# Optimization experiments

Measured on AMD Instinct MI355X. Metric: run time of the kernel, lower is better.

Reference implementation:

```python
import jax, jax.numpy as jnp
import numpy as np

GRID_LO = 32
GRID_HI = 128
NF = 4          # n_features
K = 9           # num_neighbors
NUM_CLASSES = 36
BS = 128
P_LO = GRID_LO * GRID_LO   # 1024
P_HI = GRID_HI * GRID_HI   # 16384


def _knn_neighbor_indices():
    """Replicates cKDTree(lo_coords).query(hi_coords, k=K)[1]: lo grid has
    spacing ratio=grid_hi//grid_lo, hi grid spacing 1; neighbors sorted by
    distance (stable sort -> ties broken by lower linear index)."""
    ratio = GRID_HI // GRID_LO
    lo = np.stack(np.meshgrid(np.arange(GRID_LO) * ratio,
                              np.arange(GRID_LO) * ratio, indexing='ij'),
                  axis=-1).reshape(-1, 2).astype(np.float64)   # (P_LO, 2)
    hi = np.stack(np.meshgrid(np.arange(GRID_HI),
                              np.arange(GRID_HI), indexing='ij'),
                  axis=-1).reshape(-1, 2).astype(np.float64)   # (P_HI, 2)
    d2 = ((hi[:, None, :] - lo[None, :, :]) ** 2).sum(-1)      # (P_HI, P_LO)
    idx = np.argsort(d2, axis=1, kind='stable')[:, :K]          # (P_HI, K)
    return jnp.asarray(idx, dtype=jnp.int32)


def setup_inputs() -> dict:
    key = jax.random.key(0)
    k1, k2, k3, k4, k5 = jax.random.split(key, 5)
    x = jax.random.normal(k1, (BS, NF * P_LO), dtype=jnp.float32)
    cls_ids = jax.random.randint(k2, (BS,), 0, NUM_CLASSES)
    neighbor_indices = _knn_neighbor_indices()                  # (P_HI, K)
    weight_map = jax.random.normal(k3, (NUM_CLASSES, NF, P_HI, K), dtype=jnp.float32) * 0.05
    bias_low = jax.random.normal(k4, (NUM_CLASSES, NF, P_LO), dtype=jnp.float32) * 0.05
    bias_high = jax.random.normal(k5, (NUM_CLASSES, NF, P_HI), dtype=jnp.float32) * 0.05
    return {"x": x, "cls_ids": cls_ids, "neighbor_indices": neighbor_indices,
            "weight_map": weight_map, "bias_low": bias_low, "bias_high": bias_high}


def reference(x, cls_ids, neighbor_indices, weight_map, bias_low, bias_high):
    # x: (BS, NF*P_LO) -> (BS, NF, P_LO)
    y_low = x.reshape(x.shape[0], NF, P_LO)
    y_low_db = y_low - bias_low[cls_ids]                        # (BS, NF, P_LO)
    # gather k=9 lo-res neighbors for every hi-res pixel (all features at once)
    neigh = y_low_db[:, :, neighbor_indices]                    # (BS, NF, P_HI, K)
    weights = weight_map[cls_ids]                               # (BS, NF, P_HI, K)
    out = jnp.einsum('bfpk,bfpk->bfp', neigh, weights)          # weighted sum over k
    out = out + bias_high[cls_ids]                              # (BS, NF, P_HI)
    return out.reshape(x.shape[0], NF, GRID_HI, GRID_HI)
```

## Files before the change

### kernel.cpp

```cpp
#include <hip/hip_runtime.h>

#define BS      128
#define NF      4
#define P_LO    1024
#define P_HI    16384
#define KNN     9
#define THREADS 256
#define CHUNKS  4
#define CHUNK_P (P_HI / CHUNKS)

__global__ __launch_bounds__(THREADS) void rect_up_kernel(
    const float* __restrict__ x,
    const int*   __restrict__ cls_ids,
    const int*   __restrict__ nbr,
    const float* __restrict__ wmap,
    const float* __restrict__ blo,
    const float* __restrict__ bhi,
    float*       __restrict__ out)
{
    __shared__ float ylds[P_LO];

    const int bf    = blockIdx.x / CHUNKS;
    const int chunk = blockIdx.x % CHUNKS;
    const int b     = bf >> 2;
    const int f     = bf & 3;
    const int cls   = cls_ids[b];
    const int tid   = threadIdx.x;

    const float4* xp4  = (const float4*)(x   + (b   * NF + f) * P_LO);
    const float4* blp4 = (const float4*)(blo + (cls * NF + f) * P_LO);
    {
        float4 xv = xp4[tid];
        float4 bv = blp4[tid];
        float4 r;
        r.x = xv.x - bv.x; r.y = xv.y - bv.y;
        r.z = xv.z - bv.z; r.w = xv.w - bv.w;
        ((float4*)ylds)[tid] = r;
    }
    __syncthreads();

    const float* wbase = wmap + (size_t)(cls * NF + f) * P_HI * KNN;
    const float* bhp   = bhi  + (size_t)(cls * NF + f) * P_HI;
    float*       op    = out  + (size_t)(b   * NF + f) * P_HI;

    const int pp_lo = chunk * (CHUNK_P / 2);
    const int pp_hi = pp_lo + (CHUNK_P / 2);

    #pragma unroll 4
    for (int pp = pp_lo + tid; pp < pp_hi; pp += THREADS) {
        const int p0 = pp * 2;

        const int2* ip = (const int2*)(nbr + (size_t)p0 * KNN);
        int idx[18];
        #pragma unroll
        for (int j = 0; j < 9; ++j) {
            int2 v = ip[j];
            idx[2 * j]     = v.x;
            idx[2 * j + 1] = v.y;
        }

        const float2* wp = (const float2*)(wbase + (size_t)p0 * KNN);
        float w[18];
        #pragma unroll
        for (int j = 0; j < 9; ++j) {
            float2 v = wp[j];
            w[2 * j]     = v.x;
            w[2 * j + 1] = v.y;
        }

        float acc0 = 0.f, acc1 = 0.f;
        #pragma unroll
        for (int k = 0; k < 9; ++k) acc0 = fmaf(w[k],     ylds[idx[k]],     acc0);
        #pragma unroll
        for (int k = 0; k < 9; ++k) acc1 = fmaf(w[9 + k], ylds[idx[9 + k]], acc1);

        float2 bh = *(const float2*)(bhp + p0);
        float2 o;
        o.x = acc0 + bh.x;
        o.y = acc1 + bh.y;
        *(float2*)(op + p0) = o;
    }
}

extern "C" void kernel_launch(void* const* d_in, const int* in_sizes, int n_in,
                              void* d_out, int out_size, void* d_ws, size_t ws_size,
                              hipStream_t stream) {
    const float* x    = (const float*)d_in[0];
    const int*   cls  = (const int*)d_in[1];
    const int*   nbr  = (const int*)d_in[2];
    const float* wmap = (const float*)d_in[3];
    const float* blo  = (const float*)d_in[4];
    const float* bhi  = (const float*)d_in[5];
    float*       out  = (float*)d_out;

    dim3 grid(BS * NF * CHUNKS);
    rect_up_kernel<<<grid, THREADS, 0, stream>>>(x, cls, nbr, wmap, blo, bhi, out);
}
```

Baseline: 191.6 us.

## Coalesce neighbor and weight loads via per-wave LDS product staging

Each wave now processes a tile of 128 hi-res pixels, loading the neighbor indices and weights contiguously across lanes and writing the weighted products into a per-wave LDS buffer. Each lane then reads back its two pixels' nine products and sums them. This replaces per-thread strided 72-byte loads with coalesced wave-wide accesses, targeting global memory efficiency. Chunk count doubles to give more blocks. It adds LDS traffic, possible bank conflicts on the strided readback, and a different summation order.

After: 179.4 us. 6.4% less time.

```diff
diff --git a/kernel.cpp b/kernel.cpp
--- a/kernel.cpp
+++ b/kernel.cpp
@@ -6,8 +6,11 @@
 #define P_HI    16384
 #define KNN     9
 #define THREADS 256
-#define CHUNKS  4
+#define CHUNKS  8
 #define CHUNK_P (P_HI / CHUNKS)
+#define TILE_P  128
+#define TILE_F  (TILE_P * KNN)
+#define WAVES   (THREADS / 64)
 
 __global__ __launch_bounds__(THREADS) void rect_up_kernel(
     const float* __restrict__ x,
@@ -19,6 +22,7 @@
     float*       __restrict__ out)
 {
     __shared__ float ylds[P_LO];
+    __shared__ float prod[WAVES][TILE_F];
 
     const int bf    = blockIdx.x / CHUNKS;
     const int chunk = blockIdx.x % CHUNKS;
@@ -26,10 +30,12 @@
     const int f     = bf & 3;
     const int cls   = cls_ids[b];
     const int tid   = threadIdx.x;
+    const int wave  = tid >> 6;
+    const int lane  = tid & 63;
 
-    const float4* xp4  = (const float4*)(x   + (b   * NF + f) * P_LO);
-    const float4* blp4 = (const float4*)(blo + (cls * NF + f) * P_LO);
     {
+        const float4* xp4  = (const float4*)(x   + (b   * NF + f) * P_LO);
+        const float4* blp4 = (const float4*)(blo + (cls * NF + f) * P_LO);
         float4 xv = xp4[tid];
         float4 bv = blp4[tid];
         float4 r;
@@ -42,43 +48,40 @@
     const float* wbase = wmap + (size_t)(cls * NF + f) * P_HI * KNN;
     const float* bhp   = bhi  + (size_t)(cls * NF + f) * P_HI;
     float*       op    = out  + (size_t)(b   * NF + f) * P_HI;
+    float*       pbuf  = prod[wave];
 
-    const int pp_lo = chunk * (CHUNK_P / 2);
-    const int pp_hi = pp_lo + (CHUNK_P / 2);
+    const int tiles = CHUNK_P / TILE_P;
+    for (int t = wave; t < tiles; t += WAVES) {
+        const int    ptile = chunk * CHUNK_P + t * TILE_P;
+        const size_t fbase = (size_t)ptile * KNN;
 
-    #pragma unroll 4
-    for (int pp = pp_lo + tid; pp < pp_hi; pp += THREADS) {
-        const int p0 = pp * 2;
-
-        const int2* ip = (const int2*)(nbr + (size_t)p0 * KNN);
-        int idx[18];
         #pragma unroll
-        for (int j = 0; j < 9; ++j) {
-            int2 v = ip[j];
-            idx[2 * j]     = v.x;
-            idx[2 * j + 1] = v.y;
+        for (int j = 0; j < KNN; ++j) {
+            const int off = j * 128 + 2 * lane;
+            int2   i2 = *(const int2*)  (nbr   + fbase + off);
+            float2 w2 = *(const float2*)(wbase + fbase + off);
+            float2 pr;
+            pr.x = w2.x * ylds[i2.x];
+            pr.y = w2.y * ylds[i2.y];
+            *(float2*)(pbuf + off) = pr;
         }
 
-        const float2* wp = (const float2*)(wbase + (size_t)p0 * KNN);
-        float w[18];
+        float2 r[9];
         #pragma unroll
-        for (int j = 0; j < 9; ++j) {
-            float2 v = wp[j];
-            w[2 * j]     = v.x;
-            w[2 * j + 1] = v.y;
-        }
+        for (int j = 0; j < 9; ++j)
+            r[j] = *(const float2*)(pbuf + lane * 18 + 2 * j);
 
-        float acc0 = 0.f, acc1 = 0.f;
-        #pragma unroll
-        for (int k = 0; k < 9; ++k) acc0 = fmaf(w[k],     ylds[idx[k]],     acc0);
-        #pragma unroll
-        for (int k = 0; k < 9; ++k) acc1 = fmaf(w[9 + k], ylds[idx[9 + k]], acc1);
+        float a0 = r[0].x + r[0].y + r[1].x + r[1].y + r[2].x + r[2].y
+                 + r[3].x + r[3].y + r[4].x;
+        float a1 = r[4].y + r[5].x + r[5].y + r[6].x + r[6].y
+                 + r[7].x + r[7].y + r[8].x + r[8].y;
 
-        float2 bh = *(const float2*)(bhp + p0);
+        const int pp = ptile + 2 * lane;
+        float2 bh = *(const float2*)(bhp + pp);
         float2 o;
-        o.x = acc0 + bh.x;
-        o.y = acc1 + bh.y;
-        *(float2*)(op + p0) = o;
+        o.x = a0 + bh.x;
+        o.y = a1 + bh.y;
+        *(float2*)(op + pp) = o;
     }
 }
 
```

## Group batch rows by class to reuse weight tiles across samples

Applied to the files above, without the earlier changes.

A small pre-kernel buckets batch indices by class id into workspace lists. The main kernel is then launched per (class, feature, pixel tile): it loads that tile's weights and neighbor indices into registers once and loops over every batch row of the class, double-buffering the de-biased low-res input in shared memory. This cuts repeated weight-map reads from once per sample to once per class. The cost is an extra launch, serialized per-sample iterations with a barrier each, and load imbalance or idle blocks when class counts are uneven.

Result: faster. 167.0 us (-12.8%).

```diff
diff --git a/kernel.cpp b/kernel.cpp
--- a/kernel.cpp
+++ b/kernel.cpp
@@ -2,83 +2,115 @@
 
 #define BS      128
 #define NF      4
+#define NC      36
 #define P_LO    1024
 #define P_HI    16384
 #define KNN     9
 #define THREADS 256
-#define CHUNKS  4
-#define CHUNK_P (P_HI / CHUNKS)
+#define TILE_P  512
+#define TILE_F  (TILE_P * KNN)
+#define NTILES  (P_HI / TILE_P)
+#define LIST_OFF 64
+
+__global__ __launch_bounds__(128) void build_lists_kernel(
+    const int* __restrict__ cls_ids, int* __restrict__ ws)
+{
+    __shared__ int cnt[NC];
+    const int t = threadIdx.x;
+    if (t < NC) cnt[t] = 0;
+    __syncthreads();
+    if (t < BS) {
+        int c = cls_ids[t];
+        int pos = atomicAdd(&cnt[c], 1);
+        ws[LIST_OFF + c * BS + pos] = t;
+    }
+    __syncthreads();
+    if (t < NC) ws[t] = cnt[t];
+}
 
 __global__ __launch_bounds__(THREADS) void rect_up_kernel(
     const float* __restrict__ x,
-    const int*   __restrict__ cls_ids,
+    const int*   __restrict__ ws,
     const int*   __restrict__ nbr,
     const float* __restrict__ wmap,
     const float* __restrict__ blo,
     const float* __restrict__ bhi,
     float*       __restrict__ out)
 {
-    __shared__ float ylds[P_LO];
+    __shared__ __align__(16) char smem[TILE_F * 4 * 2];
+    float* w_st = (float*)smem;
+    int*   i_st = (int*)(smem + TILE_F * 4);
+    float* ybuf = (float*)(smem + TILE_F * 4);
 
-    const int bf    = blockIdx.x / CHUNKS;
-    const int chunk = blockIdx.x % CHUNKS;
-    const int b     = bf >> 2;
-    const int f     = bf & 3;
-    const int cls   = cls_ids[b];
+    const int tile = blockIdx.x % NTILES;
+    const int cf   = blockIdx.x / NTILES;
+    const int f    = cf % NF;
+    const int cls  = cf / NF;
+
+    const int n_b = ws[cls];
+    if (n_b == 0) return;
+
     const int tid   = threadIdx.x;
+    const int tbase = tile * TILE_P;
 
-    const float4* xp4  = (const float4*)(x   + (b   * NF + f) * P_LO);
-    const float4* blp4 = (const float4*)(blo + (cls * NF + f) * P_LO);
-    {
-        float4 xv = xp4[tid];
-        float4 bv = blp4[tid];
-        float4 r;
-        r.x = xv.x - bv.x; r.y = xv.y - bv.y;
-        r.z = xv.z - bv.z; r.w = xv.w - bv.w;
-        ((float4*)ylds)[tid] = r;
+    const float4* wsrc = (const float4*)(wmap + ((size_t)(cls * NF + f) * P_HI + tbase) * KNN);
+    const int4*   isrc = (const int4*)(nbr + (size_t)tbase * KNN);
+    float4* w4 = (float4*)w_st;
+    int4*   i4 = (int4*)i_st;
+    #pragma unroll
+    for (int i = tid; i < TILE_F / 4; i += THREADS) {
+        w4[i] = wsrc[i];
+        i4[i] = isrc[i];
     }
     __syncthreads();
 
-    const float* wbase = wmap + (size_t)(cls * NF + f) * P_HI * KNN;
-    const float* bhp   = bhi  + (size_t)(cls * NF + f) * P_HI;
-    float*       op    = out  + (size_t)(b   * NF + f) * P_HI;
-
-    const int pp_lo = chunk * (CHUNK_P / 2);
-    const int pp_hi = pp_lo + (CHUNK_P / 2);
-
-    #pragma unroll 4
-    for (int pp = pp_lo + tid; pp < pp_hi; pp += THREADS) {
-        const int p0 = pp * 2;
-
-        const int2* ip = (const int2*)(nbr + (size_t)p0 * KNN);
-        int idx[18];
+    float w[18]; int nb[18];
+    {
+        const float2* wr = (const float2*)w_st + (size_t)tid * 9;
+        const int2*   ir = (const int2*)i_st + (size_t)tid * 9;
         #pragma unroll
         for (int j = 0; j < 9; ++j) {
-            int2 v = ip[j];
-            idx[2 * j]     = v.x;
-            idx[2 * j + 1] = v.y;
+            float2 a = wr[j]; w[2 * j] = a.x; w[2 * j + 1] = a.y;
+            int2   c = ir[j]; nb[2 * j] = c.x; nb[2 * j + 1] = c.y;
         }
+    }
+    __syncthreads();
 
-        const float2* wp = (const float2*)(wbase + (size_t)p0 * KNN);
-        float w[18];
+    const int    p0 = tbase + 2 * tid;
+    const float2 bh = *(const float2*)(bhi + (size_t)(cls * NF + f) * P_HI + p0);
+    const float4 bl = ((const float4*)(blo + (cls * NF + f) * P_LO))[tid];
+    const int*  list = ws + LIST_OFF + cls * BS;
+
+    {
+        const int b = list[0];
+        float4 xv = ((const float4*)(x + (b * NF + f) * P_LO))[tid];
+        float4 r;
+        r.x = xv.x - bl.x; r.y = xv.y - bl.y;
+        r.z = xv.z - bl.z; r.w = xv.w - bl.w;
+        ((float4*)ybuf)[tid] = r;
+    }
+
+    for (int s = 0; s < n_b; ++s) {
+        __syncthreads();
+        const float* y = ybuf + (s & 1) * P_LO;
+        if (s + 1 < n_b) {
+            const int b1 = list[s + 1];
+            float4 xv = ((const float4*)(x + (b1 * NF + f) * P_LO))[tid];
+            float4 r;
+            r.x = xv.x - bl.x; r.y = xv.y - bl.y;
+            r.z = xv.z - bl.z; r.w = xv.w - bl.w;
+            ((float4*)(ybuf + ((s + 1) & 1) * P_LO))[tid] = r;
+        }
+        const int b = list[s];
+        float a0 = 0.f, a1 = 0.f;
         #pragma unroll
-        for (int j = 0; j < 9; ++j) {
-            float2 v = wp[j];
-            w[2 * j]     = v.x;
-            w[2 * j + 1] = v.y;
-        }
-
-        float acc0 = 0.f, acc1 = 0.f;
+        for (int k = 0; k < 9; ++k) a0 = fmaf(w[k],     y[nb[k]],     a0);
         #pragma unroll
-        for (int k = 0; k < 9; ++k) acc0 = fmaf(w[k],     ylds[idx[k]],     acc0);
-        #pragma unroll
-        for (int k = 0; k < 9; ++k) acc1 = fmaf(w[9 + k], ylds[idx[9 + k]], acc1);
-
-        float2 bh = *(const float2*)(bhp + p0);
+        for (int k = 0; k < 9; ++k) a1 = fmaf(w[9 + k], y[nb[9 + k]], a1);
         float2 o;
-        o.x = acc0 + bh.x;
-        o.y = acc1 + bh.y;
-        *(float2*)(op + p0) = o;
+        o.x = a0 + bh.x;
+        o.y = a1 + bh.y;
+        *(float2*)(out + (size_t)(b * NF + f) * P_HI + p0) = o;
     }
 }
 
@@ -92,7 +124,9 @@
     const float* blo  = (const float*)d_in[4];
     const float* bhi  = (const float*)d_in[5];
     float*       out  = (float*)d_out;
+    int*         wsl  = (int*)d_ws;
 
-    dim3 grid(BS * NF * CHUNKS);
-    rect_up_kernel<<<grid, THREADS, 0, stream>>>(x, cls, nbr, wmap, blo, bhi, out);
+    build_lists_kernel<<<1, 128, 0, stream>>>(cls, wsl);
+    rect_up_kernel<<<NC * NF * NTILES, THREADS, 0, stream>>>(
+        x, wsl, nbr, wmap, blo, bhi, out);
 }
```
